# Performance work log

Measured on AMD Instinct MI355X. Metric: run time of the kernel, lower is better.

Reference implementation:

```python
import jax, jax.numpy as jnp
import numpy as np

EMB = 512
HEADS = 8
B, T = 8, 1024

def setup_inputs() -> dict:
    key = jax.random.key(0)
    ks = jax.random.split(key, 6)
    e, h = EMB, HEADS
    s = 1.0 / np.sqrt(e)
    x = jax.random.normal(ks[0], (B, T, e), dtype=jnp.float32)
    # Linear(emb, emb*heads, bias=False): stored as (e, e*h) for x @ W
    Wk = jax.random.normal(ks[1], (e, e * h), dtype=jnp.float32) * s
    Wq = jax.random.normal(ks[2], (e, e * h), dtype=jnp.float32) * s
    Wv = jax.random.normal(ks[3], (e, e * h), dtype=jnp.float32) * s
    # unifyheads: Linear(heads*emb, emb) with bias
    Wu = jax.random.normal(ks[4], (e * h, e), dtype=jnp.float32) * (1.0 / np.sqrt(e * h))
    bu = jax.random.normal(ks[5], (e,), dtype=jnp.float32) * 0.01
    return {"x": x, "Wk": Wk, "Wq": Wq, "Wv": Wv, "Wu": Wu, "bu": bu}

def reference(x, Wk, Wq, Wv, Wu, bu):
    b, t, e = x.shape
    h = HEADS
    scale = e ** (-0.25)  # applied to both q and k, as in the torch code
    q = (x @ Wq).reshape(b, t, h, e) * scale  # (b,t,h,e)
    k = (x @ Wk).reshape(b, t, h, e) * scale
    v = (x @ Wv).reshape(b, t, h, e)
    dot = jnp.einsum('bqhe,bkhe->bhqk', q, k)      # (b,h,t,t)
    attn = jax.nn.softmax(dot, axis=-1)
    out = jnp.einsum('bhqk,bkhe->bqhe', attn, v)    # (b,t,h,e)
    out = out.reshape(b, t, h * e)
    return out @ Wu + bu                            # (b,t,e)
```

## Files before the change

### kernel.cpp

```cpp
#include <hip/hip_runtime.h>
#include <hip/hip_bf16.h>
#include <cstdint>

typedef __attribute__((ext_vector_type(8))) short bf16x8;
typedef __attribute__((ext_vector_type(4))) float f32x4;

typedef __attribute__((address_space(1))) const void gv_t;
typedef __attribute__((address_space(3))) void lv_t;

__device__ __forceinline__ unsigned short f2b(float f) {
  __hip_bfloat16 h = __float2bfloat16(f);
  return __builtin_bit_cast(unsigned short, h);
}
__device__ __forceinline__ float b2f(unsigned short u) {
  unsigned int x = (unsigned int)u << 16;
  return __builtin_bit_cast(float, x);
}

__global__ __launch_bounds__(256) void k_cast(const float* __restrict__ src,
                                              unsigned short* __restrict__ dst, int n4) {
  int i = blockIdx.x * 256 + threadIdx.x;
  if (i >= n4) return;
  const float4 v = ((const float4*)src)[i];
  ushort4 o;
  o.x = f2b(v.x); o.y = f2b(v.y); o.z = f2b(v.z); o.w = f2b(v.w);
  ((ushort4*)dst)[i] = o;
}

__global__ void k_transpose_cast(const float* __restrict__ src,
                                 unsigned short* __restrict__ dst, int R, int C) {
  __shared__ float tile[32][33];
  const int tx = threadIdx.x, ty = threadIdx.y;
  const int c0 = blockIdx.x * 32, r0 = blockIdx.y * 32;
#pragma unroll
  for (int i = 0; i < 32; i += 8)
    tile[ty + i][tx] = src[(long)(r0 + ty + i) * C + (c0 + tx)];
  __syncthreads();
#pragma unroll
  for (int i = 0; i < 32; i += 8)
    dst[(long)(c0 + ty + i) * R + (r0 + tx)] = f2b(tile[tx][ty + i]);
}

__global__ void k_transpose_cast3(const float* __restrict__ s0, const float* __restrict__ s1,
                                  const float* __restrict__ s2,
                                  unsigned short* __restrict__ dst, int R, int C) {
  const float* src = (blockIdx.z == 0) ? s0 : ((blockIdx.z == 1) ? s1 : s2);
  unsigned short* d = dst + (size_t)blockIdx.z * R * C;
  __shared__ float tile[32][33];
  const int tx = threadIdx.x, ty = threadIdx.y;
  const int c0 = blockIdx.x * 32, r0 = blockIdx.y * 32;
#pragma unroll
  for (int i = 0; i < 32; i += 8)
    tile[ty + i][tx] = src[(long)(r0 + ty + i) * C + (c0 + tx)];
  __syncthreads();
#pragma unroll
  for (int i = 0; i < 32; i += 8)
    d[(long)(c0 + ty + i) * R + (r0 + tx)] = f2b(tile[tx][ty + i]);
}

enum { EPI_QK = 0, EPI_VT = 1 };

#define BAR256() do { asm volatile("" ::: "memory"); __builtin_amdgcn_s_barrier(); asm volatile("" ::: "memory"); } while (0)
#define WAITVM(n) do { asm volatile("s_waitcnt vmcnt(" #n ")" ::: "memory"); __builtin_amdgcn_sched_barrier(0); } while (0)
#define WAITLG() do { asm volatile("s_waitcnt lgkmcnt(0)" ::: "memory"); } while (0)

#define STAGE_A(tt, hw, qq)                                                                     \
  __builtin_amdgcn_global_load_lds(                                                            \
    (gv_t*)(A + (long)(m0 + (hw)*128 + (qq)*64 + rr) * lda + ((tt) << 6) + csw),               \
    (lv_t*)(&L[(((((tt)&1)*2 + (hw))*128 + (qq)*64 + rr))*64 + c0]), 16, 0, 0)

#define STAGE_B(tt, qi)                                                                         \
  __builtin_amdgcn_global_load_lds(                                                            \
    (gv_t*)(Bt + (long)(n0 + (qi)*64 + rr) * ldb + ((tt) << 6) + csw),                         \
    (lv_t*)(&L[32768 + (((((tt)&1)*2 + ((qi)>>1))*128 + ((qi)&1)*64 + rr))*64 + c0]), 16, 0, 0)

#define PHASE(slot, QR, QC) do {                                                                \
    const unsigned short* Abase = &L[((slot)*2 + wr) * 8192];                                   \
    const unsigned short* Bbase = &L[32768 + ((slot)*2 + (wc>>1)) * 8192];                      \
    bf16x8 afr[4][2], bfr[2][2];                                                                \
    _Pragma("unroll")                                                                           \
    for (int fr = 0; fr < 4; ++fr) {                                                            \
      const int rA = (QR)*64 + fr*16 + l15;                                                     \
      _Pragma("unroll")                                                                         \
      for (int kk = 0; kk < 2; ++kk) {                                                          \
        const int cA = (kk*32 + l4*8) ^ ((rA & 7) << 3);                                        \
        afr[fr][kk] = *(const bf16x8*)(Abase + rA*64 + cA);                                     \
      }                                                                                         \
    }                                                                                           \
    _Pragma("unroll")                                                                           \
    for (int fc = 0; fc < 2; ++fc) {                                                            \
      const int rB = (wc&1)*64 + (QC)*32 + fc*16 + l15;                                         \
      _Pragma("unroll")                                                                         \
      for (int kk = 0; kk < 2; ++kk) {                                                          \
        const int cB = (kk*32 + l4*8) ^ ((rB & 7) << 3);                                        \
        bfr[fc][kk] = *(const bf16x8*)(Bbase + rB*64 + cB);                                     \
      }                                                                                         \
    }                                                                                           \
    __builtin_amdgcn_s_setprio(1);                                                              \
    _Pragma("unroll")                                                                           \
    for (int fr = 0; fr < 4; ++fr)                                                              \
      _Pragma("unroll")                                                                         \
      for (int fc = 0; fc < 2; ++fc)                                                            \
        _Pragma("unroll")                                                                       \
        for (int kk = 0; kk < 2; ++kk)                                                          \
          acc[(QR)*4+fr][(QC)*2+fc] = __builtin_amdgcn_mfma_f32_16x16x32_bf16(                  \
              afr[fr][kk], bfr[fc][kk], acc[(QR)*4+fr][(QC)*2+fc], 0, 0, 0);                    \
    __builtin_amdgcn_s_setprio(0);                                                              \
  } while (0)

template <int EPI>
__global__ __launch_bounds__(512)
void k_gemm256(const unsigned short* __restrict__ A, const unsigned short* __restrict__ Bt,
               void* __restrict__ Cv, int K, int lda, int ldb, float scale) {
  const int m0 = blockIdx.y * 256;
  const int n0 = blockIdx.x * 256;
  __shared__ __align__(16) unsigned short L[65536];
  const int tid = threadIdx.x;
  const int lane = tid & 63;
  const int wid = tid >> 6;
  const int wr = wid >> 2;
  const int wc = wid & 3;
  const int l15 = lane & 15;
  const int l4 = lane >> 4;
  const int rr = tid >> 3;
  const int c0 = (tid & 7) * 8;
  const int csw = c0 ^ ((rr & 7) << 3);

  f32x4 acc[8][4] = {};
  const int NT = K >> 6;

  STAGE_A(0, 0, 0); STAGE_A(0, 1, 0); STAGE_A(0, 0, 1); STAGE_A(0, 1, 1);
  STAGE_B(0, 0); STAGE_B(0, 1); STAGE_B(0, 2); STAGE_B(0, 3);
  if (NT > 1) {
    STAGE_A(1, 0, 0); STAGE_A(1, 1, 0);
    WAITVM(2);
  } else {
    WAITVM(0);
  }
  __builtin_amdgcn_s_barrier();
  asm volatile("" ::: "memory");

  for (int t = 0; t < NT; ++t) {
    const int slot = t & 1;
    if (t + 1 < NT) { STAGE_A(t + 1, 0, 1); STAGE_A(t + 1, 1, 1); }
    PHASE(slot, 0, 0);
    BAR256();
    if (t + 1 < NT) { STAGE_B(t + 1, 0); STAGE_B(t + 1, 1); }
    PHASE(slot, 0, 1);
    BAR256();
    if (t + 1 < NT) { STAGE_B(t + 1, 2); STAGE_B(t + 1, 3); }
    if (t + 2 < NT) { STAGE_A(t + 2, 0, 0); STAGE_A(t + 2, 1, 0); }
    PHASE(slot, 1, 0);
    BAR256();
    PHASE(slot, 1, 1);
    if (t + 1 < NT) {
      if (t + 2 < NT) WAITVM(2);
      else            WAITVM(0);
      __builtin_amdgcn_s_barrier();
      asm volatile("" ::: "memory");
    }
  }

#pragma unroll
  for (int i = 0; i < 8; ++i) {
#pragma unroll
    for (int j = 0; j < 4; ++j) {
#pragma unroll
      for (int r = 0; r < 4; ++r) {
        const int row = m0 + wr * 128 + i * 16 + l4 * 4 + r;
        const int col = n0 + wc * 64 + j * 16 + l15;
        const float v = acc[i][j][r];
        if (EPI == EPI_QK) {
          unsigned short* o = (unsigned short*)Cv;
          const int sec = col >> 12;
          const int cc = col & 4095;
          const long addr = (long)sec * 33554432 +
              ((long)((row >> 10) * 8 + (cc >> 9)) * 1024 + (row & 1023)) * 512 + (cc & 511);
          o[addr] = f2b(v * scale);
        } else {
          unsigned short* o = (unsigned short*)Cv;
          const long addr = (long)((col >> 10) * 8 + (row >> 9)) * 524288 +
                            (long)(row & 511) * 1024 + (col & 1023);
          o[addr] = f2b(v);
        }
      }
    }
  }
}

#define KLD 520
#define VGRP 544

__device__ __forceinline__ void stage_k(const unsigned short* kg, unsigned short* dst,
                                        int c, int w, int lane) {
#pragma unroll
  for (int i = 0; i < 4; ++i) {
    const int row = i * 8 + w;
    __builtin_amdgcn_global_load_lds(
        (gv_t*)(kg + (size_t)(c * 32 + row) * 512 + lane * 8),
        (lv_t*)(dst + row * KLD + lane * 8), 16, 0, 0);
  }
}
__device__ __forceinline__ void stage_v(const unsigned short* vg, unsigned short* dst,
                                        int c, int w, int lane) {
#pragma unroll
  for (int i = 0; i < 4; ++i) {
    const int G = i * 8 + w;
    const int e = G * 16 + (lane >> 2);
    __builtin_amdgcn_global_load_lds(
        (gv_t*)(vg + (size_t)e * 1024 + c * 32 + (lane & 3) * 8),
        (lv_t*)(dst + G * VGRP + lane * 8), 16, 0, 0);
  }
}

__global__ __launch_bounds__(512)
void k_attn(unsigned short* __restrict__ q,
            const unsigned short* __restrict__ k,
            const unsigned short* __restrict__ vt)
{
  __shared__ __align__(16) unsigned short Ks[2][32 * KLD];
  __shared__ __align__(16) unsigned short Vs[2][32 * VGRP];
  __shared__ __align__(16) unsigned short Es[2][2560];
  const int bid = blockIdx.x;
  const int head = (bid & 7) * 8 + ((bid >> 3) >> 4);
  const int qt = (bid >> 3) & 15;
  const int tid = threadIdx.x;
  const int w = tid >> 6, lane = tid & 63;
  const int l15 = lane & 15, l4 = lane >> 4;
  const int qf = w & 3, kf = w >> 2;

  unsigned short* qg = q + (size_t)(head * 1024 + qt * 64) * 512;
  const unsigned short* kg = k + (size_t)head * 524288;
  const unsigned short* vg = vt + (size_t)head * 524288;

  const int qrow = qf * 16 + l15;
  const int krow = kf * 16 + l15;

  bf16x8 q_r[16];
#pragma unroll
  for (int ks = 0; ks < 16; ++ks)
    q_r[ks] = *(const bf16x8*)(qg + (size_t)qrow * 512 + (size_t)(ks * 4 + l4) * 8);

  stage_k(kg, &Ks[0][0], 0, w, lane);
  stage_v(vg, &Vs[0][0], 0, w, lane);
  stage_k(kg, &Ks[1][0], 1, w, lane);

  f32x4 acc[4][4] = {};
  float partial = 0.f;
  const int erow = tid >> 3;
  const int ej = tid & 7;
  const int eidx = 40 * erow + ej * 4;

  for (int c = 0; c < 32; ++c) {
    unsigned short* KsC = &Ks[c & 1][0];
    unsigned short* VsC = &Vs[c & 1][0];
    unsigned short* EsC = &Es[c & 1][0];
    if (c < 31) { WAITVM(4); } else { WAITVM(0); }
    WAITLG();
    __builtin_amdgcn_s_barrier();
    asm volatile("" ::: "memory");
    if (c + 1 < 32) stage_v(vg, &Vs[(c + 1) & 1][0], c + 1, w, lane);
    f32x4 sacc0 = {0.f, 0.f, 0.f, 0.f};
    f32x4 sacc1 = {0.f, 0.f, 0.f, 0.f};
    __builtin_amdgcn_s_setprio(1);
#pragma unroll
    for (int ks = 0; ks < 16; ks += 2) {
      bf16x8 bk0 = *(const bf16x8*)(&KsC[krow * KLD + (ks * 4 + l4) * 8]);
      sacc0 = __builtin_amdgcn_mfma_f32_16x16x32_bf16(q_r[ks], bk0, sacc0, 0, 0, 0);
      bf16x8 bk1 = *(const bf16x8*)(&KsC[krow * KLD + ((ks + 1) * 4 + l4) * 8]);
      sacc1 = __builtin_amdgcn_mfma_f32_16x16x32_bf16(q_r[ks + 1], bk1, sacc1, 0, 0, 0);
    }
    __builtin_amdgcn_s_setprio(0);
#pragma unroll
    for (int r = 0; r < 4; ++r) {
      const int qq = qf * 16 + l4 * 4 + r;
      const int kk2 = kf * 16 + l15;
      EsC[40 * qq + kk2] = f2b(__expf(sacc0[r] + sacc1[r]));
    }
    WAITLG();
    __builtin_amdgcn_s_barrier();
    asm volatile("" ::: "memory");
    if (c + 2 < 32) stage_k(kg, KsC, c + 2, w, lane);
    {
      const ushort4 ev = *(const ushort4*)(&EsC[eidx]);
      partial += (b2f(ev.x) + b2f(ev.y)) + (b2f(ev.z) + b2f(ev.w));
    }
    bf16x8 bv[4];
#pragma unroll
    for (int cf = 0; cf < 4; ++cf) {
      const int G = w * 4 + cf;
      bv[cf] = *(const bf16x8*)(&VsC[G * VGRP + l15 * 32 + l4 * 8]);
    }
    __builtin_amdgcn_s_setprio(1);
#pragma unroll
    for (int qf2 = 0; qf2 < 4; ++qf2) {
      const int qq = qf2 * 16 + l15;
      bf16x8 ae = *(const bf16x8*)(&EsC[40 * qq + 8 * l4]);
#pragma unroll
      for (int cf = 0; cf < 4; ++cf)
        acc[qf2][cf] = __builtin_amdgcn_mfma_f32_16x16x32_bf16(ae, bv[cf], acc[qf2][cf], 0, 0, 0);
    }
    __builtin_amdgcn_s_setprio(0);
  }

  __syncthreads();
  float* fs = (float*)&Ks[0][0];
  fs[tid] = partial;
  __syncthreads();
  if (tid < 64) {
    float s = 0.f;
#pragma unroll
    for (int j = 0; j < 8; ++j) s += fs[tid * 8 + j];
    fs[512 + tid] = 1.0f / s;
  }
  __syncthreads();

#pragma unroll
  for (int qf2 = 0; qf2 < 4; ++qf2) {
#pragma unroll
    for (int r = 0; r < 4; ++r) {
      const int qq = qf2 * 16 + l4 * 4 + r;
      const float iv = fs[512 + qq];
#pragma unroll
      for (int cf = 0; cf < 4; ++cf) {
        const int e = (w * 4 + cf) * 16 + l15;
        qg[(size_t)qq * 512 + e] = f2b(acc[qf2][cf][r] * iv);
      }
    }
  }
}

__global__ __launch_bounds__(256)
void k_gemm_out(const unsigned short* __restrict__ A, const unsigned short* __restrict__ Bt,
                float* __restrict__ C, const float* __restrict__ bias) {
  const int m0 = blockIdx.y * 128;
  const int n0 = blockIdx.x * 128;
  __shared__ __align__(16) unsigned short As[2][128 * 32];
  __shared__ __align__(16) unsigned short Bs[2][128 * 32];
  const int tid = threadIdx.x;
  const int lane = tid & 63;
  const int wm = ((tid >> 6) >> 1) * 64;
  const int wn = ((tid >> 6) & 1) * 64;
  const int srow = tid >> 2;
  const int scol = (tid & 3) * 8;
  f32x4 acc[4][4] = {};

  const int row1 = m0 + srow, row2 = row1 + 64;
  const size_t hb1 = (size_t)(row1 >> 10) * 8 * 524288 + (size_t)(row1 & 1023) * 512;
  const size_t hb2 = (size_t)(row2 >> 10) * 8 * 524288 + (size_t)(row2 & 1023) * 512;
  const unsigned short* gb = Bt + (size_t)(n0 + srow) * 4096 + scol;

#define STAGEO(buf, k0) do {                                                                          \
    const size_t koffA = (size_t)((k0) >> 9) * 524288 + ((k0) & 511) + scol;                          \
    __builtin_amdgcn_global_load_lds((gv_t*)(A + hb1 + koffA), (lv_t*)(&As[buf][tid * 8]), 16, 0, 0);  \
    __builtin_amdgcn_global_load_lds((gv_t*)(A + hb2 + koffA), (lv_t*)(&As[buf][tid * 8 + 2048]), 16, 0, 0); \
    __builtin_amdgcn_global_load_lds((gv_t*)(gb + (k0)), (lv_t*)(&Bs[buf][tid * 8]), 16, 0, 0);        \
    __builtin_amdgcn_global_load_lds((gv_t*)(gb + 64L * 4096 + (k0)), (lv_t*)(&Bs[buf][tid * 8 + 2048]), 16, 0, 0); \
  } while (0)

  STAGEO(0, 0);
  for (int k0 = 0; k0 < 4096; k0 += 32) {
    const int cur = (k0 >> 5) & 1;
    __syncthreads();
    if (k0 + 32 < 4096) { STAGEO(cur ^ 1, k0 + 32); }
    const unsigned short* ap = &As[cur][(wm + (lane & 15)) * 32 + (lane >> 4) * 8];
    const unsigned short* bp = &Bs[cur][(wn + (lane & 15)) * 32 + (lane >> 4) * 8];
    bf16x8 fa[4], fb[4];
#pragma unroll
    for (int i = 0; i < 4; ++i) fa[i] = *(const bf16x8*)(ap + i * 16 * 32);
#pragma unroll
    for (int i = 0; i < 4; ++i) fb[i] = *(const bf16x8*)(bp + i * 16 * 32);
#pragma unroll
    for (int mi = 0; mi < 4; ++mi)
#pragma unroll
      for (int ni = 0; ni < 4; ++ni)
        acc[mi][ni] = __builtin_amdgcn_mfma_f32_16x16x32_bf16(fa[mi], fb[ni], acc[mi][ni], 0, 0, 0);
  }
#undef STAGEO

#pragma unroll
  for (int mi = 0; mi < 4; ++mi) {
#pragma unroll
    for (int ni = 0; ni < 4; ++ni) {
#pragma unroll
      for (int r = 0; r < 4; ++r) {
        const int row = m0 + wm + mi * 16 + ((lane >> 4) * 4 + r);
        const int col = n0 + wn + ni * 16 + (lane & 15);
        C[(long)row * 512 + col] = acc[mi][ni][r] + bias[col];
      }
    }
  }
}

extern "C" void kernel_launch(void* const* d_in, const int* in_sizes, int n_in,
                              void* d_out, int out_size, void* d_ws, size_t ws_size,
                              hipStream_t stream) {
  const float* x  = (const float*)d_in[0];
  const float* Wk = (const float*)d_in[1];
  const float* Wq = (const float*)d_in[2];
  const float* Wv = (const float*)d_in[3];
  const float* Wu = (const float*)d_in[4];
  const float* bu = (const float*)d_in[5];
  float* out = (float*)d_out;
  char* ws = (char*)d_ws;

  const size_t NEED = 226492416;
  if (ws_size < NEED) return;

  unsigned short* wut   = (unsigned short*)(ws + 0);
  unsigned short* wtqkv = (unsigned short*)(ws + 4194304);
  unsigned short* xb    = (unsigned short*)(ws + 16777216);
  unsigned short* qb    = (unsigned short*)(ws + 25165824);
  unsigned short* kb    = qb + 33554432;
  unsigned short* vtb   = qb + 67108864;

  const float s4 = 0.21022410381342865f;

  k_cast<<<4096, 256, 0, stream>>>(x, xb, 1048576);
  k_transpose_cast3<<<dim3(128, 16, 3), dim3(32, 8), 0, stream>>>(Wq, Wk, Wv, wtqkv, 512, 4096);
  k_transpose_cast<<<dim3(16, 128), dim3(32, 8), 0, stream>>>(Wu, wut, 4096, 512);

  k_gemm256<EPI_QK><<<dim3(32, 32, 1), 512, 0, stream>>>(xb, wtqkv, qb, 512, 512, 512, s4);
  k_gemm256<EPI_VT><<<dim3(32, 16, 1), 512, 0, stream>>>(wtqkv + 4194304, xb, vtb, 512, 512, 512, 1.0f);

  k_attn<<<1024, 512, 0, stream>>>(qb, kb, vtb);

  k_gemm_out<<<dim3(4, 64, 1), 256, 0, stream>>>(qb, wut, out, bu);
}
```

Baseline: 466.8 us.

## Widen attention key chunk to 64 and load V fragments directly from global

The attention kernel now processes 64 keys per iteration instead of 32, which halves the loop trips and barriers. Each wave computes two 16-row Q fragments against one K fragment, so every K load from LDS feeds two MFMAs, and the K-dimension split that needed summing partial scores is gone. V is no longer staged through LDS: each wave reads its V^T fragments straight from global memory into registers. In exchange, more Q registers are kept live, the K tile in LDS grows, and global V loads sit on the critical path of each iteration.

```diff
diff --git a/kernel.cpp b/kernel.cpp
--- a/kernel.cpp
+++ b/kernel.cpp
@@ -189,27 +189,16 @@
 }
 
 #define KLD 520
-#define VGRP 544
-
-__device__ __forceinline__ void stage_k(const unsigned short* kg, unsigned short* dst,
-                                        int c, int w, int lane) {
-#pragma unroll
-  for (int i = 0; i < 4; ++i) {
+#define ELD 72
+
+__device__ __forceinline__ void stage_k64(const unsigned short* kg, unsigned short* dst,
+                                          int c, int w, int lane) {
+#pragma unroll
+  for (int i = 0; i < 8; ++i) {
     const int row = i * 8 + w;
     __builtin_amdgcn_global_load_lds(
-        (gv_t*)(kg + (size_t)(c * 32 + row) * 512 + lane * 8),
+        (gv_t*)(kg + (size_t)(c * 64 + row) * 512 + lane * 8),
         (lv_t*)(dst + row * KLD + lane * 8), 16, 0, 0);
-  }
-}
-__device__ __forceinline__ void stage_v(const unsigned short* vg, unsigned short* dst,
-                                        int c, int w, int lane) {
-#pragma unroll
-  for (int i = 0; i < 4; ++i) {
-    const int G = i * 8 + w;
-    const int e = G * 16 + (lane >> 2);
-    __builtin_amdgcn_global_load_lds(
-        (gv_t*)(vg + (size_t)e * 1024 + c * 32 + (lane & 3) * 8),
-        (lv_t*)(dst + G * VGRP + lane * 8), 16, 0, 0);
   }
 }
 
@@ -218,87 +207,94 @@
             const unsigned short* __restrict__ k,
             const unsigned short* __restrict__ vt)
 {
-  __shared__ __align__(16) unsigned short Ks[2][32 * KLD];
-  __shared__ __align__(16) unsigned short Vs[2][32 * VGRP];
-  __shared__ __align__(16) unsigned short Es[2][2560];
+  __shared__ __align__(16) unsigned short Ks[2][64 * KLD];
+  __shared__ __align__(16) unsigned short Es[2][64 * ELD];
   const int bid = blockIdx.x;
   const int head = (bid & 7) * 8 + ((bid >> 3) >> 4);
   const int qt = (bid >> 3) & 15;
   const int tid = threadIdx.x;
   const int w = tid >> 6, lane = tid & 63;
   const int l15 = lane & 15, l4 = lane >> 4;
-  const int qf = w & 3, kf = w >> 2;
+  const int qf = w & 1;
+  const int kf = w >> 1;
 
   unsigned short* qg = q + (size_t)(head * 1024 + qt * 64) * 512;
   const unsigned short* kg = k + (size_t)head * 524288;
   const unsigned short* vg = vt + (size_t)head * 524288;
 
-  const int qrow = qf * 16 + l15;
   const int krow = kf * 16 + l15;
 
-  bf16x8 q_r[16];
-#pragma unroll
-  for (int ks = 0; ks < 16; ++ks)
-    q_r[ks] = *(const bf16x8*)(qg + (size_t)qrow * 512 + (size_t)(ks * 4 + l4) * 8);
-
-  stage_k(kg, &Ks[0][0], 0, w, lane);
-  stage_v(vg, &Vs[0][0], 0, w, lane);
-  stage_k(kg, &Ks[1][0], 1, w, lane);
+  bf16x8 q_r[2][16];
+#pragma unroll
+  for (int j = 0; j < 2; ++j)
+#pragma unroll
+    for (int ks = 0; ks < 16; ++ks)
+      q_r[j][ks] = *(const bf16x8*)(qg + (size_t)(qf * 32 + j * 16 + l15) * 512 +
+                                    (size_t)(ks * 4 + l4) * 8);
+
+  stage_k64(kg, &Ks[0][0], 0, w, lane);
+  stage_k64(kg, &Ks[1][0], 1, w, lane);
+  WAITVM(8);
+  __builtin_amdgcn_s_barrier();
+  asm volatile("" ::: "memory");
 
   f32x4 acc[4][4] = {};
   float partial = 0.f;
-  const int erow = tid >> 3;
-  const int ej = tid & 7;
-  const int eidx = 40 * erow + ej * 4;
-
-  for (int c = 0; c < 32; ++c) {
+
+  for (int c = 0; c < 16; ++c) {
     unsigned short* KsC = &Ks[c & 1][0];
-    unsigned short* VsC = &Vs[c & 1][0];
     unsigned short* EsC = &Es[c & 1][0];
-    if (c < 31) { WAITVM(4); } else { WAITVM(0); }
+    if (c) {
+      if (c < 15) { WAITVM(8); } else { WAITVM(0); }
+      __builtin_amdgcn_s_barrier();
+      asm volatile("" ::: "memory");
+    }
+    bf16x8 bv[4][2];
+#pragma unroll
+    for (int cf = 0; cf < 4; ++cf)
+#pragma unroll
+      for (int h = 0; h < 2; ++h)
+        bv[cf][h] = *(const bf16x8*)(vg + (size_t)(w * 64 + cf * 16 + l15) * 1024 +
+                                     c * 64 + h * 32 + l4 * 8);
+    __builtin_amdgcn_sched_barrier(0);
+    f32x4 s0 = {0.f, 0.f, 0.f, 0.f};
+    f32x4 s1 = {0.f, 0.f, 0.f, 0.f};
+    __builtin_amdgcn_s_setprio(1);
+#pragma unroll
+    for (int ks = 0; ks < 16; ++ks) {
+      bf16x8 bk = *(const bf16x8*)(&KsC[krow * KLD + (ks * 4 + l4) * 8]);
+      s0 = __builtin_amdgcn_mfma_f32_16x16x32_bf16(q_r[0][ks], bk, s0, 0, 0, 0);
+      s1 = __builtin_amdgcn_mfma_f32_16x16x32_bf16(q_r[1][ks], bk, s1, 0, 0, 0);
+    }
+    __builtin_amdgcn_s_setprio(0);
+#pragma unroll
+    for (int r = 0; r < 4; ++r) {
+      const int q0 = qf * 32 + l4 * 4 + r;
+      EsC[q0 * ELD + kf * 16 + l15] = f2b(__expf(s0[r]));
+      EsC[(q0 + 16) * ELD + kf * 16 + l15] = f2b(__expf(s1[r]));
+    }
     WAITLG();
     __builtin_amdgcn_s_barrier();
     asm volatile("" ::: "memory");
-    if (c + 1 < 32) stage_v(vg, &Vs[(c + 1) & 1][0], c + 1, w, lane);
-    f32x4 sacc0 = {0.f, 0.f, 0.f, 0.f};
-    f32x4 sacc1 = {0.f, 0.f, 0.f, 0.f};
-    __builtin_amdgcn_s_setprio(1);
-#pragma unroll
-    for (int ks = 0; ks < 16; ks += 2) {
-      bf16x8 bk0 = *(const bf16x8*)(&KsC[krow * KLD + (ks * 4 + l4) * 8]);
-      sacc0 = __builtin_amdgcn_mfma_f32_16x16x32_bf16(q_r[ks], bk0, sacc0, 0, 0, 0);
-      bf16x8 bk1 = *(const bf16x8*)(&KsC[krow * KLD + ((ks + 1) * 4 + l4) * 8]);
-      sacc1 = __builtin_amdgcn_mfma_f32_16x16x32_bf16(q_r[ks + 1], bk1, sacc1, 0, 0, 0);
-    }
-    __builtin_amdgcn_s_setprio(0);
-#pragma unroll
-    for (int r = 0; r < 4; ++r) {
-      const int qq = qf * 16 + l4 * 4 + r;
-      const int kk2 = kf * 16 + l15;
-      EsC[40 * qq + kk2] = f2b(__expf(sacc0[r] + sacc1[r]));
-    }
-    WAITLG();
-    __builtin_amdgcn_s_barrier();
-    asm volatile("" ::: "memory");
-    if (c + 2 < 32) stage_k(kg, KsC, c + 2, w, lane);
+    if (c + 2 < 16) stage_k64(kg, KsC, c + 2, w, lane);
     {
-      const ushort4 ev = *(const ushort4*)(&EsC[eidx]);
-      partial += (b2f(ev.x) + b2f(ev.y)) + (b2f(ev.z) + b2f(ev.w));
-    }
-    bf16x8 bv[4];
-#pragma unroll
-    for (int cf = 0; cf < 4; ++cf) {
-      const int G = w * 4 + cf;
-      bv[cf] = *(const bf16x8*)(&VsC[G * VGRP + l15 * 32 + l4 * 8]);
+      const int row = tid >> 3;
+      const ushort4* p = (const ushort4*)(&EsC[row * ELD + (tid & 7) * 8]);
+      const ushort4 a = p[0], b = p[1];
+      partial += ((b2f(a.x) + b2f(a.y)) + (b2f(a.z) + b2f(a.w))) +
+                 ((b2f(b.x) + b2f(b.y)) + (b2f(b.z) + b2f(b.w)));
     }
     __builtin_amdgcn_s_setprio(1);
 #pragma unroll
     for (int qf2 = 0; qf2 < 4; ++qf2) {
       const int qq = qf2 * 16 + l15;
-      bf16x8 ae = *(const bf16x8*)(&EsC[40 * qq + 8 * l4]);
-#pragma unroll
-      for (int cf = 0; cf < 4; ++cf)
-        acc[qf2][cf] = __builtin_amdgcn_mfma_f32_16x16x32_bf16(ae, bv[cf], acc[qf2][cf], 0, 0, 0);
+      bf16x8 ae0 = *(const bf16x8*)(&EsC[qq * ELD + l4 * 8]);
+      bf16x8 ae1 = *(const bf16x8*)(&EsC[qq * ELD + 32 + l4 * 8]);
+#pragma unroll
+      for (int cf = 0; cf < 4; ++cf) {
+        acc[qf2][cf] = __builtin_amdgcn_mfma_f32_16x16x32_bf16(ae0, bv[cf][0], acc[qf2][cf], 0, 0, 0);
+        acc[qf2][cf] = __builtin_amdgcn_mfma_f32_16x16x32_bf16(ae1, bv[cf][1], acc[qf2][cf], 0, 0, 0);
+      }
     }
     __builtin_amdgcn_s_setprio(0);
   }
@@ -323,7 +319,7 @@
       const float iv = fs[512 + qq];
 #pragma unroll
       for (int cf = 0; cf < 4; ++cf) {
-        const int e = (w * 4 + cf) * 16 + l15;
+        const int e = w * 64 + cf * 16 + l15;
         qg[(size_t)qq * 512 + e] = f2b(acc[qf2][cf][r] * iv);
       }
     }
```

New measurement: 526.1 us. 12.7% more time.
